# Performance work log

Hardware: AMD Instinct MI355X
Metric: run time of the kernel (lower is better)

The kernel has to match this reference:

```python
import jax, jax.numpy as jnp
import numpy as np

NA = 131072
DG = 150          # GRU hidden size
DS = 50           # static context dim
DIN = 12          # decoding_steps * 2
VEL_CONST = 0.5


def setup_inputs() -> dict:
    key = jax.random.key(0)
    ks = jax.random.split(key, 18)
    s = 0.1  # weight init scale keeps exp(apd_2) numerically tame
    inp = {
        "z": jax.random.normal(ks[0], (NA, 2), jnp.float32),
        "x_flat": jax.random.normal(ks[1], (NA, DIN), jnp.float32),
        "h": jax.random.normal(ks[2], (1, NA, DG), jnp.float32),
        "static": jax.random.normal(ks[3], (NA, DS), jnp.float32),
        "dx": jax.random.normal(ks[4], (NA, 2), jnp.float32),
        "x_prev": jax.random.normal(ks[5], (NA, 2), jnp.float32),
        # GRU params (torch layout: gates ordered r, z, n; shape [3*DG, in])
        "W_ih": jax.random.normal(ks[6], (3 * DG, DIN), jnp.float32) * s,
        "W_hh": jax.random.normal(ks[7], (3 * DG, DG), jnp.float32) * s,
        "b_ih": jax.random.normal(ks[8], (3 * DG,), jnp.float32) * s,
        "b_hh": jax.random.normal(ks[9], (3 * DG,), jnp.float32) * s,
        # MLP: Linear(200,50) -> Softplus -> Linear(50,50) -> Tanh -> Linear(50,6)
        "W1": jax.random.normal(ks[10], (50, DG + DS), jnp.float32) * s,
        "b1": jax.random.normal(ks[11], (50,), jnp.float32) * s,
        "W2": jax.random.normal(ks[12], (50, 50), jnp.float32) * s,
        "b2": jax.random.normal(ks[13], (50,), jnp.float32) * s,
        "W3": jax.random.normal(ks[14], (6, 50), jnp.float32) * s,
        "b3": jax.random.normal(ks[15], (6,), jnp.float32) * s,
    }
    return inp


def _gru_cell(x, h0, W_ih, W_hh, b_ih, b_hh):
    # torch GRU single step. x: [Na, DIN], h0: [Na, DG]
    gx = x @ W_ih.T + b_ih          # [Na, 3*DG]
    gh = h0 @ W_hh.T + b_hh         # [Na, 3*DG]
    xr, xz, xn = jnp.split(gx, 3, axis=-1)
    hr, hz, hn = jnp.split(gh, 3, axis=-1)
    r = jax.nn.sigmoid(xr + hr)
    zg = jax.nn.sigmoid(xz + hz)
    n = jnp.tanh(xn + r * hn)
    return (1.0 - zg) * n + zg * h0


def reference(z, x_flat, h, static, dx, x_prev,
              W_ih, W_hh, b_ih, b_hh, W1, b1, W2, b2, W3, b3):
    h_new = _gru_cell(x_flat, h[0], W_ih, W_hh, b_ih, b_hh)  # [Na, DG]
    dyn_static = jnp.concatenate([h_new, static], axis=-1)    # [Na, DG+DS]
    hmlp = jax.nn.softplus(dyn_static @ W1.T + b1)
    hmlp = jnp.tanh(hmlp @ W2.T + b2)
    out = hmlp @ W3.T + b3                                    # [Na, 6]

    mu_hat = out[:, :2]
    sh = out[:, 2:].reshape(-1, 2, 2)                         # sigma_hat
    mu = x_prev + VEL_CONST * dx + mu_hat

    b = sh[:, 0, 1] + sh[:, 1, 0]
    apd_2 = sh[:, 0, 0] + sh[:, 1, 1]
    amd_2 = sh[:, 0, 0] - sh[:, 1, 1]
    delta = jnp.sqrt(amd_2 ** 2 + b ** 2)
    sinh = jnp.sinh(delta)
    cosh = jnp.cosh(delta)
    tmp1 = sinh / delta
    tmp2 = amd_2 / tmp1
    s00 = cosh + tmp2
    s01 = b * tmp1
    s11 = cosh - tmp2
    sigma = jnp.stack([jnp.stack([s00, s01], axis=-1),
                       jnp.stack([s01, s11], axis=-1)], axis=-2)  # [Na,2,2]
    sigma = sigma * jnp.exp(apd_2)[:, None, None]

    x = jnp.einsum('nij,nj->ni', sigma, z) + mu
    return x, mu, sigma, h_new[None]
```

## Files before the change

kernel.cpp:

```cpp
#include <hip/hip_runtime.h>
#include <math.h>

#define NA 131072
#define NBLK (NA/64)

typedef __bf16 bf16x8 __attribute__((ext_vector_type(8)));
typedef float f32x16 __attribute__((ext_vector_type(16)));

#define APACK_OFF 0
#define BIAS4_OFF 214016
#define W1P_OFF   216448
#define W2P_OFF   243072

__device__ __forceinline__ unsigned short f2b(float f){
  __bf16 h = (__bf16)f;
  unsigned short u;
  __builtin_memcpy(&u, &h, 2);
  return u;
}
__device__ __forceinline__ float b2f(unsigned short u){
  unsigned x = ((unsigned)u) << 16; float f;
  __builtin_memcpy(&f, &x, 4); return f;
}
__device__ __forceinline__ bf16x8 asb(uint4 u){ return __builtin_bit_cast(bf16x8, u); }
__device__ __forceinline__ f32x16 mfma32(bf16x8 a, bf16x8 b, f32x16 c){
  return __builtin_amdgcn_mfma_f32_32x32x16_bf16(a, b, c, 0, 0, 0);
}
__device__ __forceinline__ float fsigmoid(float x){ return 1.f/(1.f+__expf(-x)); }
__device__ __forceinline__ float ftanh(float x){ return 1.f - 2.f/(__expf(2.f*x)+1.f); }

__global__ __launch_bounds__(256) void prep2(
    const float* __restrict__ W_ih, const float* __restrict__ W_hh,
    const float* __restrict__ b_ih, const float* __restrict__ b_hh,
    const float* __restrict__ W1, const float* __restrict__ W2,
    float* __restrict__ ws)
{
  int tid = blockIdx.x*blockDim.x + threadIdx.x;
  int stride = gridDim.x*blockDim.x;
  unsigned short* Ap  = (unsigned short*)((char*)ws + APACK_OFF);
  float*          B4  = (float*)((char*)ws + BIAS4_OFF);
  unsigned short* W1p = (unsigned short*)((char*)ws + W1P_OFF);
  unsigned short* W2p = (unsigned short*)((char*)ws + W2P_OFF);

  for (int s = tid; s < 19*11*64; s += stride){
    int lane = s & 63; int t2 = s >> 6; int ks = t2 % 11; int mt = t2 / 11;
    int R = mt*32 + (lane & 31);
    int kb = ks*16 + (lane >> 5)*8;
    int j = R >> 2, g = R & 3;
    #pragma unroll
    for (int i=0;i<8;i++){
      int k = kb + i; float f = 0.f;
      if (j < 150){
        if (k < 12){
          if (g==0) f = W_ih[j*12+k];
          else if (g==1) f = W_ih[(150+j)*12+k];
          else if (g==3) f = W_ih[(300+j)*12+k];
        } else if (k >= 16 && k < 166){
          int kh = k - 16;
          if (g==0) f = W_hh[j*150+kh];
          else if (g==1) f = W_hh[(150+j)*150+kh];
          else if (g==2) f = W_hh[(300+j)*150+kh];
        }
      }
      Ap[s*8+i] = f2b(f);
    }
  }
  for (int j = tid; j < 152; j += stride){
    float4 bv = make_float4(0.f,0.f,0.f,0.f);
    if (j < 150){
      bv.x = b_ih[j]       + b_hh[j];
      bv.y = b_ih[150+j]   + b_hh[150+j];
      bv.z = b_hh[300+j];
      bv.w = b_ih[300+j];
    }
    ((float4*)B4)[j] = bv;
  }
  for (int s = tid; s < 2*13*64; s += stride){
    int lane = s & 63; int t2 = s >> 6; int ks = t2 % 13; int mt = t2 / 13;
    int o = mt*32 + (lane & 31);
    int kb = ks*16 + (lane >> 5)*8;
    #pragma unroll
    for (int i=0;i<8;i++){
      int k = kb + i;
      float f = (o < 50 && k < 200) ? W1[o*200+k] : 0.f;
      W1p[s*8+i] = f2b(f);
    }
  }
  for (int s = tid; s < 2*4*64; s += stride){
    int lane = s & 63; int t2 = s >> 6; int ks = t2 % 4; int mt = t2 / 4;
    int o = mt*32 + (lane & 31);
    int kb = ks*16 + (lane >> 5)*8;
    #pragma unroll
    for (int i=0;i<8;i++){
      int k = kb + i;
      float f = (o < 50 && k < 50) ? W2[o*50+k] : 0.f;
      W2p[s*8+i] = f2b(f);
    }
  }
}

__global__ __launch_bounds__(256,4) void fused_kernel(
    const float* __restrict__ x_flat, const float* __restrict__ h_in,
    const float* __restrict__ st, const float* __restrict__ z_in,
    const float* __restrict__ dx, const float* __restrict__ xp,
    const float* __restrict__ b1, const float* __restrict__ b2,
    const float* __restrict__ W3, const float* __restrict__ b3,
    const unsigned short* __restrict__ Apack, const float* __restrict__ Bias4,
    const unsigned short* __restrict__ W1p, const unsigned short* __restrict__ W2p,
    float* __restrict__ out)
{
  __shared__ char smem[36864];
  unsigned short* sm_ag = (unsigned short*)smem;
  unsigned short* sm_xf = (unsigned short*)(smem + 27648);
  unsigned short* sm_h1 = (unsigned short*)(smem + 27648);
  float*          sm_h2 = (float*)smem;
  unsigned*       ag32  = (unsigned*)sm_ag;

  int t = threadIdx.x; int lane = t & 63; int w = t >> 6;
  int hi = lane >> 5, cl = lane & 31;
  long ab = (long)blockIdx.x * 64;

  const float2* h2p = (const float2*)h_in;
  for (int s = t; s < 4800; s += 256){
    int a = s/75, k2 = s - a*75;
    float2 v = h2p[ab*75 + s];
    ag32[a*108 + k2] = (unsigned)f2b(v.x) | ((unsigned)f2b(v.y) << 16);
  }
  const float2* s2p = (const float2*)st;
  for (int s = t; s < 1600; s += 256){
    int a = s/25, k2 = s - a*25;
    float2 v = s2p[ab*25 + s];
    ag32[a*108 + 75 + k2] = (unsigned)f2b(v.x) | ((unsigned)f2b(v.y) << 16);
  }
  for (int s = t; s < 512; s += 256)
    ag32[(s>>3)*108 + 100 + (s&7)] = 0u;
  for (int s = t; s < 1024; s += 256){
    int nt2 = s >> 9; int r = s & 511; int ln = r >> 3; int i = r & 7;
    int k = ((ln >> 5) << 3) + i;
    int agent = nt2*32 + (ln & 31);
    unsigned short v = 0;
    if (k < 12) v = f2b(x_flat[(ab+agent)*12 + k]);
    sm_xf[s] = v;
  }
  __syncthreads();

  bf16x8 B0[11], B1[11];
  {
    B0[0] = asb(((const uint4*)sm_xf)[lane]);
    B1[0] = asb(((const uint4*)sm_xf)[64 + lane]);
    const uint4* r0 = (const uint4*)(sm_ag + cl*216);
    const uint4* r1 = (const uint4*)(sm_ag + (32+cl)*216);
    #pragma unroll
    for (int ks=1; ks<11; ks++){
      B0[ks] = asb(r0[(ks-1)*2 + hi]);
      B1[ks] = asb(r1[(ks-1)*2 + hi]);
    }
  }
  __syncthreads();

  for (int s = t; s < 2304; s += 256) ((unsigned*)sm_h1)[s] = 0u;

  const uint4* ApV = (const uint4*)Apack;
  #pragma unroll 1
  for (int mt = w; mt < 19; mt += 4){
    f32x16 acc0;
    #pragma unroll
    for (int q=0;q<4;q++){
      float4 bq = ((const float4*)Bias4)[mt*8 + 2*q + hi];
      acc0[4*q+0]=bq.x; acc0[4*q+1]=bq.y; acc0[4*q+2]=bq.z; acc0[4*q+3]=bq.w;
    }
    f32x16 acc1 = acc0;
    const uint4* ap = ApV + (size_t)(mt*11)*64 + lane;
    #pragma unroll
    for (int ks=0; ks<11; ks++){
      bf16x8 af = asb(ap[ks*64]);
      acc0 = mfma32(af, B0[ks], acc0);
      acc1 = mfma32(af, B1[ks], acc1);
    }
    #pragma unroll
    for (int nt=0; nt<2; nt++){
      const f32x16& acc = nt ? acc1 : acc0;
      int a = nt*32 + cl;
      #pragma unroll
      for (int q=0;q<4;q++){
        int j = mt*8 + 2*q + hi;
        if (j < 150){
          float h0 = b2f(sm_ag[a*216 + j]);
          float r = fsigmoid(acc[4*q+0]);
          float z = fsigmoid(acc[4*q+1]);
          float n = ftanh(acc[4*q+3] + r*acc[4*q+2]);
          sm_ag[a*216 + j] = f2b(n + z*(h0 - n));
        }
      }
    }
  }
  __syncthreads();

  float2* oh2 = (float2*)(out + (size_t)8*NA);
  for (int s = t; s < 4800; s += 256){
    int a = s/75, k2 = s - a*75;
    unsigned u = ag32[a*108 + k2];
    float2 v; v.x = b2f((unsigned short)u); v.y = b2f((unsigned short)(u>>16));
    oh2[ab*75 + s] = v;
  }

  int mt2 = w >> 1; int a2 = (w & 1)*32 + cl;
  f32x16 acc;
  #pragma unroll
  for (int r=0;r<16;r++){
    int o = mt2*32 + (r&3) + 8*(r>>2) + 4*hi;
    acc[r] = (o < 50) ? b1[o] : 0.f;
  }
  {
    const uint4* rv  = (const uint4*)(sm_ag + a2*216);
    const uint4* w1v = (const uint4*)W1p;
    #pragma unroll
    for (int ks=0; ks<13; ks++){
      acc = mfma32(asb(w1v[(mt2*13+ks)*64 + lane]), asb(rv[ks*2+hi]), acc);
    }
  }
  #pragma unroll
  for (int r=0;r<16;r++){
    int o = mt2*32 + (r&3) + 8*(r>>2) + 4*hi;
    if (o < 50){
      float xx = acc[r];
      float spv = fmaxf(xx,0.f) + __logf(1.f + __expf(-fabsf(xx)));
      sm_h1[a2*72 + o] = f2b(spv);
    }
  }
  __syncthreads();

  f32x16 acc2;
  #pragma unroll
  for (int r=0;r<16;r++){
    int o = mt2*32 + (r&3) + 8*(r>>2) + 4*hi;
    acc2[r] = (o < 50) ? b2[o] : 0.f;
  }
  {
    const uint4* r1v = (const uint4*)(sm_h1 + a2*72);
    const uint4* w2v = (const uint4*)W2p;
    #pragma unroll
    for (int ks=0; ks<4; ks++){
      acc2 = mfma32(asb(w2v[(mt2*4+ks)*64 + lane]), asb(r1v[ks*2+hi]), acc2);
    }
  }
  #pragma unroll
  for (int r=0;r<16;r++){
    int o = mt2*32 + (r&3) + 8*(r>>2) + 4*hi;
    if (o < 50) sm_h2[a2*51 + o] = ftanh(acc2[r]);
  }
  __syncthreads();

  if (t < 64){
    int a = t; long ga = ab + a;
    float o6[6];
    #pragma unroll
    for (int jj=0;jj<6;jj++) o6[jj] = b3[jj];
    for (int k=0;k<50;k++){
      float v = sm_h2[a*51 + k];
      #pragma unroll
      for (int jj=0;jj<6;jj++) o6[jj] = fmaf(v, W3[jj*50+k], o6[jj]);
    }
    float mu0 = xp[ga*2+0] + 0.5f*dx[ga*2+0] + o6[0];
    float mu1 = xp[ga*2+1] + 0.5f*dx[ga*2+1] + o6[1];
    float bb  = o6[3] + o6[4];
    float apd = o6[2] + o6[5];
    float amd = o6[2] - o6[5];
    float delta = sqrtf(amd*amd + bb*bb);
    float e  = __expf(delta);
    float ei = 1.f/e;
    float sinh_ = 0.5f*(e - ei);
    float cosh_ = 0.5f*(e + ei);
    float tmp1 = sinh_/delta;
    float tmp2 = amd/tmp1;
    float ea = __expf(apd);
    float s00 = (cosh_+tmp2)*ea;
    float s01 = (bb*tmp1)*ea;
    float s11 = (cosh_-tmp2)*ea;
    float z0 = z_in[ga*2+0], z1 = z_in[ga*2+1];
    out[ga*2+0] = s00*z0 + s01*z1 + mu0;
    out[ga*2+1] = s01*z0 + s11*z1 + mu1;
    out[(size_t)2*NA + ga*2+0] = mu0;
    out[(size_t)2*NA + ga*2+1] = mu1;
    out[(size_t)4*NA + ga*4+0] = s00;
    out[(size_t)4*NA + ga*4+1] = s01;
    out[(size_t)4*NA + ga*4+2] = s01;
    out[(size_t)4*NA + ga*4+3] = s11;
  }
}

extern "C" void kernel_launch(void* const* d_in, const int* in_sizes, int n_in,
                              void* d_out, int out_size, void* d_ws, size_t ws_size,
                              hipStream_t stream) {
  const float* z      = (const float*)d_in[0];
  const float* x_flat = (const float*)d_in[1];
  const float* h      = (const float*)d_in[2];
  const float* st     = (const float*)d_in[3];
  const float* dx     = (const float*)d_in[4];
  const float* xp     = (const float*)d_in[5];
  const float* W_ih   = (const float*)d_in[6];
  const float* W_hh   = (const float*)d_in[7];
  const float* b_ih   = (const float*)d_in[8];
  const float* b_hh   = (const float*)d_in[9];
  const float* W1     = (const float*)d_in[10];
  const float* b1     = (const float*)d_in[11];
  const float* W2     = (const float*)d_in[12];
  const float* b2     = (const float*)d_in[13];
  const float* W3     = (const float*)d_in[14];
  const float* b3     = (const float*)d_in[15];
  float* out = (float*)d_out;
  float* ws  = (float*)d_ws;

  const unsigned short* Apack = (const unsigned short*)((char*)ws + APACK_OFF);
  const float*          Bias4 = (const float*)((char*)ws + BIAS4_OFF);
  const unsigned short* W1p   = (const unsigned short*)((char*)ws + W1P_OFF);
  const unsigned short* W2p   = (const unsigned short*)((char*)ws + W2P_OFF);

  hipLaunchKernelGGL(prep2, dim3(128), dim3(256), 0, stream,
                     W_ih, W_hh, b_ih, b_hh, W1, W2, ws);
  hipLaunchKernelGGL(fused_kernel, dim3(NBLK), dim3(256), 0, stream,
                     x_flat, h, st, z, dx, xp, b1, b2, W3, b3,
                     Apack, Bias4, W1p, W2p, out);
}
```

Before: 123.3 us.

## Halve agents per block to 32, dropping second MFMA column tile

Each block now handles 32 agents instead of 64, so twice as many blocks launch. LDS use per block halves and the second B operand set and accumulator go away, which should free registers and raise occupancy. In exchange, each Apack weight fragment loaded from global or L2 now feeds only one MFMA instead of two, doubling weight traffic per agent. Only two of the four waves do work in the MLP stages, and the final stage is handled by half a wave.

```diff
diff --git a/kernel.cpp b/kernel.cpp
--- a/kernel.cpp
+++ b/kernel.cpp
@@ -2,7 +2,7 @@
 #include <math.h>
 
 #define NA 131072
-#define NBLK (NA/64)
+#define NBLK32 (NA/32)
 
 typedef __bf16 bf16x8 __attribute__((ext_vector_type(8)));
 typedef float f32x16 __attribute__((ext_vector_type(16)));
@@ -109,56 +109,52 @@
     const unsigned short* __restrict__ W1p, const unsigned short* __restrict__ W2p,
     float* __restrict__ out)
 {
-  __shared__ char smem[36864];
+  __shared__ char smem[18432];
   unsigned short* sm_ag = (unsigned short*)smem;
-  unsigned short* sm_xf = (unsigned short*)(smem + 27648);
-  unsigned short* sm_h1 = (unsigned short*)(smem + 27648);
+  unsigned short* sm_xf = (unsigned short*)(smem + 13824);
+  unsigned short* sm_h1 = (unsigned short*)(smem + 13824);
   float*          sm_h2 = (float*)smem;
   unsigned*       ag32  = (unsigned*)sm_ag;
 
   int t = threadIdx.x; int lane = t & 63; int w = t >> 6;
   int hi = lane >> 5, cl = lane & 31;
-  long ab = (long)blockIdx.x * 64;
+  long ab = (long)blockIdx.x * 32;
 
   const float2* h2p = (const float2*)h_in;
-  for (int s = t; s < 4800; s += 256){
+  for (int s = t; s < 2400; s += 256){
     int a = s/75, k2 = s - a*75;
     float2 v = h2p[ab*75 + s];
     ag32[a*108 + k2] = (unsigned)f2b(v.x) | ((unsigned)f2b(v.y) << 16);
   }
   const float2* s2p = (const float2*)st;
-  for (int s = t; s < 1600; s += 256){
+  for (int s = t; s < 800; s += 256){
     int a = s/25, k2 = s - a*25;
     float2 v = s2p[ab*25 + s];
     ag32[a*108 + 75 + k2] = (unsigned)f2b(v.x) | ((unsigned)f2b(v.y) << 16);
   }
-  for (int s = t; s < 512; s += 256)
-    ag32[(s>>3)*108 + 100 + (s&7)] = 0u;
-  for (int s = t; s < 1024; s += 256){
-    int nt2 = s >> 9; int r = s & 511; int ln = r >> 3; int i = r & 7;
+  if (t < 256){
+    int s = t;
+    if (s < 256) ag32[(s>>3)*108 + 100 + (s&7)] = 0u;
+  }
+  for (int s = t; s < 512; s += 256){
+    int ln = s >> 3; int i = s & 7;
     int k = ((ln >> 5) << 3) + i;
-    int agent = nt2*32 + (ln & 31);
+    int agent = ln & 31;
     unsigned short v = 0;
     if (k < 12) v = f2b(x_flat[(ab+agent)*12 + k]);
     sm_xf[s] = v;
   }
   __syncthreads();
 
-  bf16x8 B0[11], B1[11];
-  {
-    B0[0] = asb(((const uint4*)sm_xf)[lane]);
-    B1[0] = asb(((const uint4*)sm_xf)[64 + lane]);
-    const uint4* r0 = (const uint4*)(sm_ag + cl*216);
-    const uint4* r1 = (const uint4*)(sm_ag + (32+cl)*216);
-    #pragma unroll
-    for (int ks=1; ks<11; ks++){
-      B0[ks] = asb(r0[(ks-1)*2 + hi]);
-      B1[ks] = asb(r1[(ks-1)*2 + hi]);
-    }
-  }
-  __syncthreads();
-
-  for (int s = t; s < 2304; s += 256) ((unsigned*)sm_h1)[s] = 0u;
+  const uint4* xfv = (const uint4*)sm_xf;
+  const uint4* r0v = (const uint4*)(sm_ag + cl*216);
+  bf16x8 B0[11];
+  B0[0] = asb(xfv[lane]);
+  #pragma unroll
+  for (int ks=1; ks<11; ks++) B0[ks] = asb(r0v[(ks-1)*2 + hi]);
+  __syncthreads();
+
+  for (int s = t; s < 1152; s += 256) ((unsigned*)sm_h1)[s] = 0u;
 
   const uint4* ApV = (const uint4*)Apack;
   #pragma unroll 1
@@ -169,89 +165,86 @@
       float4 bq = ((const float4*)Bias4)[mt*8 + 2*q + hi];
       acc0[4*q+0]=bq.x; acc0[4*q+1]=bq.y; acc0[4*q+2]=bq.z; acc0[4*q+3]=bq.w;
     }
-    f32x16 acc1 = acc0;
     const uint4* ap = ApV + (size_t)(mt*11)*64 + lane;
     #pragma unroll
     for (int ks=0; ks<11; ks++){
-      bf16x8 af = asb(ap[ks*64]);
-      acc0 = mfma32(af, B0[ks], acc0);
-      acc1 = mfma32(af, B1[ks], acc1);
-    }
-    #pragma unroll
-    for (int nt=0; nt<2; nt++){
-      const f32x16& acc = nt ? acc1 : acc0;
-      int a = nt*32 + cl;
-      #pragma unroll
-      for (int q=0;q<4;q++){
-        int j = mt*8 + 2*q + hi;
-        if (j < 150){
-          float h0 = b2f(sm_ag[a*216 + j]);
-          float r = fsigmoid(acc[4*q+0]);
-          float z = fsigmoid(acc[4*q+1]);
-          float n = ftanh(acc[4*q+3] + r*acc[4*q+2]);
-          sm_ag[a*216 + j] = f2b(n + z*(h0 - n));
-        }
+      acc0 = mfma32(asb(ap[ks*64]), B0[ks], acc0);
+    }
+    int a = cl;
+    #pragma unroll
+    for (int q=0;q<4;q++){
+      int j = mt*8 + 2*q + hi;
+      if (j < 150){
+        float h0 = b2f(sm_ag[a*216 + j]);
+        float r = fsigmoid(acc0[4*q+0]);
+        float z = fsigmoid(acc0[4*q+1]);
+        float n = ftanh(acc0[4*q+3] + r*acc0[4*q+2]);
+        sm_ag[a*216 + j] = f2b(n + z*(h0 - n));
       }
     }
   }
   __syncthreads();
 
   float2* oh2 = (float2*)(out + (size_t)8*NA);
-  for (int s = t; s < 4800; s += 256){
-    int a = s/75, k2 = s - a*75;
-    unsigned u = ag32[a*108 + k2];
+  for (int s = t; s < 2400; s += 256){
+    unsigned u = ag32[(s/75)*108 + (s - (s/75)*75)];
     float2 v; v.x = b2f((unsigned short)u); v.y = b2f((unsigned short)(u>>16));
     oh2[ab*75 + s] = v;
   }
 
-  int mt2 = w >> 1; int a2 = (w & 1)*32 + cl;
-  f32x16 acc;
-  #pragma unroll
-  for (int r=0;r<16;r++){
-    int o = mt2*32 + (r&3) + 8*(r>>2) + 4*hi;
-    acc[r] = (o < 50) ? b1[o] : 0.f;
-  }
-  {
-    const uint4* rv  = (const uint4*)(sm_ag + a2*216);
-    const uint4* w1v = (const uint4*)W1p;
-    #pragma unroll
-    for (int ks=0; ks<13; ks++){
-      acc = mfma32(asb(w1v[(mt2*13+ks)*64 + lane]), asb(rv[ks*2+hi]), acc);
-    }
-  }
-  #pragma unroll
-  for (int r=0;r<16;r++){
-    int o = mt2*32 + (r&3) + 8*(r>>2) + 4*hi;
-    if (o < 50){
-      float xx = acc[r];
-      float spv = fmaxf(xx,0.f) + __logf(1.f + __expf(-fabsf(xx)));
-      sm_h1[a2*72 + o] = f2b(spv);
-    }
-  }
-  __syncthreads();
-
-  f32x16 acc2;
-  #pragma unroll
-  for (int r=0;r<16;r++){
-    int o = mt2*32 + (r&3) + 8*(r>>2) + 4*hi;
-    acc2[r] = (o < 50) ? b2[o] : 0.f;
-  }
-  {
-    const uint4* r1v = (const uint4*)(sm_h1 + a2*72);
-    const uint4* w2v = (const uint4*)W2p;
-    #pragma unroll
-    for (int ks=0; ks<4; ks++){
-      acc2 = mfma32(asb(w2v[(mt2*4+ks)*64 + lane]), asb(r1v[ks*2+hi]), acc2);
-    }
-  }
-  #pragma unroll
-  for (int r=0;r<16;r++){
-    int o = mt2*32 + (r&3) + 8*(r>>2) + 4*hi;
-    if (o < 50) sm_h2[a2*51 + o] = ftanh(acc2[r]);
-  }
-  __syncthreads();
-
-  if (t < 64){
+  if (w < 2){
+    int mt2 = w;
+    f32x16 acc;
+    #pragma unroll
+    for (int r=0;r<16;r++){
+      int o = mt2*32 + (r&3) + 8*(r>>2) + 4*hi;
+      acc[r] = (o < 50) ? b1[o] : 0.f;
+    }
+    {
+      const uint4* rv  = (const uint4*)(sm_ag + cl*216);
+      const uint4* w1v = (const uint4*)W1p;
+      #pragma unroll
+      for (int ks=0; ks<13; ks++){
+        acc = mfma32(asb(w1v[(mt2*13+ks)*64 + lane]), asb(rv[ks*2+hi]), acc);
+      }
+    }
+    #pragma unroll
+    for (int r=0;r<16;r++){
+      int o = mt2*32 + (r&3) + 8*(r>>2) + 4*hi;
+      if (o < 50){
+        float xx = acc[r];
+        float spv = fmaxf(xx,0.f) + __logf(1.f + __expf(-fabsf(xx)));
+        sm_h1[cl*72 + o] = f2b(spv);
+      }
+    }
+  }
+  __syncthreads();
+
+  if (w < 2){
+    int mt2 = w;
+    f32x16 acc2;
+    #pragma unroll
+    for (int r=0;r<16;r++){
+      int o = mt2*32 + (r&3) + 8*(r>>2) + 4*hi;
+      acc2[r] = (o < 50) ? b2[o] : 0.f;
+    }
+    {
+      const uint4* r1v = (const uint4*)(sm_h1 + cl*72);
+      const uint4* w2v = (const uint4*)W2p;
+      #pragma unroll
+      for (int ks=0; ks<4; ks++){
+        acc2 = mfma32(asb(w2v[(mt2*4+ks)*64 + lane]), asb(r1v[ks*2+hi]), acc2);
+      }
+    }
+    #pragma unroll
+    for (int r=0;r<16;r++){
+      int o = mt2*32 + (r&3) + 8*(r>>2) + 4*hi;
+      if (o < 50) sm_h2[cl*51 + o] = ftanh(acc2[r]);
+    }
+  }
+  __syncthreads();
+
+  if (t < 32){
     int a = t; long ga = ab + a;
     float o6[6];
     #pragma unroll
@@ -318,7 +311,7 @@
 
   hipLaunchKernelGGL(prep2, dim3(128), dim3(256), 0, stream,
                      W_ih, W_hh, b_ih, b_hh, W1, W2, ws);
-  hipLaunchKernelGGL(fused_kernel, dim3(NBLK), dim3(256), 0, stream,
+  hipLaunchKernelGGL(fused_kernel, dim3(NBLK32), dim3(256), 0, stream,
                      x_flat, h, st, z, dx, xp, b1, b2, W3, b3,
                      Apack, Bias4, W1p, W2p, out);
 }
```

Result: faster. 109.6 us (-11.2%).
